# Kernel tuning notes

Hardware: AMD Instinct MI355X
Metric: run time of the kernel (lower is better)

## Reference

```python
import jax, jax.numpy as jnp
import numpy as np

# Single-device simulation of MoE down-proj GEMM + intra-node reduce-scatter.
# Leading axis R simulates the tensor-parallel ranks (K-shards); summing over R
# is the reduce part of the reduce-scatter.

def setup_inputs() -> dict:
    key = jax.random.key(0)
    k1, k2, k3, k4 = jax.random.split(key, 4)
    R, T, TOPK, Kp, E, H = 4, 2048, 2, 1024, 8, 4096
    intermediate_states = jax.random.normal(k1, (R, T * TOPK, Kp), dtype=jnp.float16)
    w = (jax.random.normal(k2, (R, E, Kp, H), dtype=jnp.float16) * jnp.float16(0.02))
    topk_ids = jax.random.randint(k3, (T, TOPK), 0, E, dtype=jnp.int32)
    tw = jax.random.uniform(k4, (T, TOPK), dtype=jnp.float32)
    topk_weight = tw / tw.sum(axis=-1, keepdims=True)
    return {"intermediate_states": intermediate_states, "w": w,
            "topk_ids": topk_ids, "topk_weight": topk_weight}


def reference(intermediate_states, w, topk_ids, topk_weight):
    # intermediate_states: [R, T*TOPK, Kp] fp16 (per-rank K-shard of expert act.)
    # w:                   [R, E, Kp, H]   fp16 (per-rank shard of down-proj)
    # topk_ids:            [T, TOPK] int32 expert assignment per token slot
    # topk_weight:         [T, TOPK] fp32  router weights
    R, MT, Kp = intermediate_states.shape
    E, H = w.shape[1], w.shape[3]
    T, TOPK = topk_ids.shape
    ids = topk_ids.reshape(-1)  # [MT]
    zero = jnp.zeros((), intermediate_states.dtype)
    acc = jnp.zeros((MT, H), dtype=jnp.float32)
    # Grouped GEMM expressed as dense masked GEMMs (E is small & fixed);
    # sum over r == reduce over tensor-parallel K-shards (reduce-scatter).
    for r in range(R):
        for e in range(E):
            xm = jnp.where((ids == e)[:, None], intermediate_states[r], zero)
            acc = acc + jnp.matmul(xm, w[r, e], preferred_element_type=jnp.float32)
    acc = acc * topk_weight.reshape(-1)[:, None]          # router weighting
    out = acc.reshape(T, TOPK, H).sum(axis=1)              # reduce topk per token
    return out.astype(intermediate_states.dtype)           # [T, H] fp16
```

## Files before the change

### kernel.cpp

```cpp
#include <hip/hip_runtime.h>
#include <stdint.h>

#define R_    4
#define T_    2048
#define TOPK_ 2
#define MT_   (T_ * TOPK_)
#define Kp_   1024
#define E_    8
#define H_    4096

#define BM 128
#define BN 128
#define BK 64
#define NKI 64
#define MAXT 40
#define NWG  (MAXT * (H_ / BN))

#define WS_TE    16
#define WS_TRS   80
#define WS_TNR   144
#define WS_RIDX  256
#define WS_X16_OFF   32768
#define WS_X16_BYTES ((size_t)R_ * MT_ * Kp_ * 2)
#define WS_NEEDED    (WS_X16_OFF + WS_X16_BYTES)

typedef _Float16 f16x8 __attribute__((ext_vector_type(8)));
typedef __fp16   h16x2 __attribute__((ext_vector_type(2)));
typedef float    f32x4 __attribute__((ext_vector_type(4)));
typedef float    f32x2 __attribute__((ext_vector_type(2)));

__device__ __forceinline__ void gload_lds16(const void* g, void* l) {
  __builtin_amdgcn_global_load_lds(
      (const __attribute__((address_space(1))) uint8_t*)g,
      (__attribute__((address_space(3))) uint8_t*)l, 16, 0, 0);
}

__global__ void moe_prep(const int* __restrict__ ids, int* __restrict__ ws) {
  __shared__ int cnt[E_], off[E_], cur[E_];
  const int tid = threadIdx.x;
  if (tid < E_) { cnt[tid] = 0; cur[tid] = 0; }
  __syncthreads();
  for (int m = tid; m < MT_; m += 256) atomicAdd(&cnt[ids[m]], 1);
  __syncthreads();
  if (tid == 0) {
    int o = 0, nt = 0;
    for (int e = 0; e < E_; ++e) {
      off[e] = o;
      int c = cnt[e];
      for (int t = 0; t < (c + 127) / 128; ++t) {
        ws[WS_TE + nt]  = e;
        ws[WS_TRS + nt] = o + t * 128;
        int rem = c - t * 128;
        ws[WS_TNR + nt] = rem < 128 ? rem : 128;
        ++nt;
      }
      o += c;
    }
    for (; nt < MAXT; ++nt) ws[WS_TNR + nt] = 0;
  }
  __syncthreads();
  for (int m = tid; m < MT_; m += 256) {
    int e = ids[m];
    int p = off[e] + atomicAdd(&cur[e], 1);
    ws[WS_RIDX + p] = m;
  }
}

__global__ void cvt_x(const float* __restrict__ x, _Float16* __restrict__ x16) {
  const size_t n = (size_t)R_ * MT_ * Kp_;
  size_t i = ((size_t)blockIdx.x * 256 + threadIdx.x) * 8;
  const size_t stride = (size_t)gridDim.x * 256 * 8;
  for (; i < n; i += stride) {
    f32x4 a = *(const f32x4*)(x + i);
    f32x4 b = *(const f32x4*)(x + i + 4);
    union { f16x8 v; h16x2 h[4]; } u;
    u.h[0] = __builtin_amdgcn_cvt_pkrtz(a[0], a[1]);
    u.h[1] = __builtin_amdgcn_cvt_pkrtz(a[2], a[3]);
    u.h[2] = __builtin_amdgcn_cvt_pkrtz(b[0], b[1]);
    u.h[3] = __builtin_amdgcn_cvt_pkrtz(b[2], b[3]);
    *(f16x8*)(x16 + i) = u.v;
  }
}

__global__ __launch_bounds__(512, 4) void moe_gemm_f(
    const _Float16* __restrict__ x16, const float* __restrict__ w,
    const float* __restrict__ tw, const int* __restrict__ ws,
    float* __restrict__ out)
{
  __shared__ __align__(16) char Alds[2][16384];
  __shared__ __align__(16) char Blds[2][16384];

  const int lid = blockIdx.x;
  const int swz = (lid & 7) * (NWG / 8) + (lid >> 3);
  const int bt  = swz % MAXT;
  const int h0  = (swz / MAXT) * BN;

  const int nr = ws[WS_TNR + bt];
  if (nr == 0) return;
  const int e  = ws[WS_TE + bt];
  const int rs = ws[WS_TRS + bt];
  const int* __restrict__ ridx = ws + WS_RIDX;

  const int tid = threadIdx.x;
  const int wv  = tid >> 6;
  const int ln  = tid & 63;
  const int g   = ln >> 4;
  const int c16 = ln & 15;
  const int wr = wv >> 2, wc = wv & 3;

  uint32_t asrc[2];
#pragma unroll
  for (int i = 0; i < 2; ++i) {
    int q   = tid * 16 + i * 8192;
    int row = q >> 7;
    int col = (q & 127) ^ (((q >> 7) & 7) << 4);
    int rcl = row < nr ? row : nr - 1;
    asrc[i] = (uint32_t)ridx[rs + rcl] * (Kp_ * 2) + col;
  }

  const int p  = tid & 63;
  const int kh = tid >> 6;
  const int hr0 = 2 * p, hr1 = 2 * p + 1;
  const uint32_t bw0 = hr0 * 128 + ((kh * 16) ^ ((hr0 & 7) << 4));
  const uint32_t bw1 = hr1 * 128 + ((kh * 16) ^ ((hr1 & 7) << 4));

  uint32_t aoff[4][2], boff[2][2];
#pragma unroll
  for (int mi = 0; mi < 4; ++mi) {
    int row = wr * 64 + mi * 16 + c16;
#pragma unroll
    for (int ks = 0; ks < 2; ++ks)
      aoff[mi][ks] = row * 128 + ((ks * 64 + g * 16) ^ ((row & 7) << 4));
  }
#pragma unroll
  for (int ni = 0; ni < 2; ++ni) {
    int row = wc * 32 + ni * 16 + c16;
#pragma unroll
    for (int ks = 0; ks < 2; ++ks)
      boff[ni][ks] = row * 128 + ((ks * 64 + g * 16) ^ ((row & 7) << 4));
  }

  f32x4 acc[4][2];
#pragma unroll
  for (int mi = 0; mi < 4; ++mi)
#pragma unroll
    for (int ni = 0; ni < 2; ++ni)
      acc[mi][ni] = f32x4{0.f, 0.f, 0.f, 0.f};

  const char* xb = (const char*)x16;
  f32x2 bvE[8], bvO[8];

#define AISSUE(BUF_, KK_) do {                                              \
    const int r_ = (KK_) >> 4, kb_ = ((KK_) & 15) << 7;                     \
    const char* xk_ = xb + (size_t)r_ * (MT_ * Kp_ * 2) + kb_;              \
    _Pragma("unroll")                                                       \
    for (int i_ = 0; i_ < 2; ++i_)                                          \
      gload_lds16(xk_ + asrc[i_], Alds[BUF_] + i_ * 8192 + wv * 1024);      \
  } while (0)

#define BISSUE(BV_, KK_) do {                                               \
    const int r_ = (KK_) >> 4, kp_ = ((KK_) & 15) << 6;                     \
    const float* wk_ = w + (((size_t)(r_ * E_ + e)) * Kp_ + kp_) * H_ + h0; \
    _Pragma("unroll")                                                       \
    for (int i_ = 0; i_ < 8; ++i_)                                          \
      BV_[i_] = *(const f32x2*)(wk_ + (size_t)(kh * 8 + i_) * H_ + 2 * p);  \
  } while (0)

#define BWRITE(BV_, BUF_) do {                                              \
    union { f16x8 v; h16x2 h[4]; } lo_, hi_;                                \
    _Pragma("unroll")                                                       \
    for (int j_ = 0; j_ < 4; ++j_) {                                        \
      lo_.h[j_] = __builtin_amdgcn_cvt_pkrtz(BV_[2*j_][0], BV_[2*j_+1][0]); \
      hi_.h[j_] = __builtin_amdgcn_cvt_pkrtz(BV_[2*j_][1], BV_[2*j_+1][1]); \
    }                                                                       \
    *(f16x8*)(Blds[BUF_] + bw0) = lo_.v;                                    \
    *(f16x8*)(Blds[BUF_] + bw1) = hi_.v;                                    \
  } while (0)

#define COMPUTE_KS(BUF_, KS_) do {                                          \
    f16x8 af[4], bf[2];                                                     \
    _Pragma("unroll")                                                       \
    for (int mi = 0; mi < 4; ++mi)                                          \
      af[mi] = *(const f16x8*)(Alds[BUF_] + aoff[mi][KS_]);                 \
    _Pragma("unroll")                                                       \
    for (int ni = 0; ni < 2; ++ni)                                          \
      bf[ni] = *(const f16x8*)(Blds[BUF_] + boff[ni][KS_]);                 \
    __builtin_amdgcn_s_setprio(1);                                          \
    _Pragma("unroll")                                                       \
    for (int mi = 0; mi < 4; ++mi)                                          \
      _Pragma("unroll")                                                     \
      for (int ni = 0; ni < 2; ++ni)                                        \
        acc[mi][ni] = __builtin_amdgcn_mfma_f32_16x16x32_f16(               \
            af[mi], bf[ni], acc[mi][ni], 0, 0, 0);                          \
    __builtin_amdgcn_s_setprio(0);                                          \
  } while (0)

  BISSUE(bvE, 0);
  AISSUE(0, 0);
  BWRITE(bvE, 0);
  BISSUE(bvO, 1);
  asm volatile("s_waitcnt vmcnt(8)" ::: "memory");
  asm volatile("s_waitcnt lgkmcnt(0)" ::: "memory");
  __builtin_amdgcn_s_barrier();

  for (int kk = 0; kk <= NKI - 4; kk += 2) {
    __builtin_amdgcn_sched_barrier(0);
    COMPUTE_KS(0, 0);
    AISSUE(1, kk + 1);
    BISSUE(bvE, kk + 2);
    __builtin_amdgcn_sched_barrier(0);
    BWRITE(bvO, 1);
    COMPUTE_KS(0, 1);
    asm volatile("s_waitcnt vmcnt(8)" ::: "memory");
    asm volatile("s_waitcnt lgkmcnt(0)" ::: "memory");
    __builtin_amdgcn_s_barrier();
    __builtin_amdgcn_sched_barrier(0);
    COMPUTE_KS(1, 0);
    AISSUE(0, kk + 2);
    BISSUE(bvO, kk + 3);
    __builtin_amdgcn_sched_barrier(0);
    BWRITE(bvE, 0);
    COMPUTE_KS(1, 1);
    asm volatile("s_waitcnt vmcnt(8)" ::: "memory");
    asm volatile("s_waitcnt lgkmcnt(0)" ::: "memory");
    __builtin_amdgcn_s_barrier();
  }
  __builtin_amdgcn_sched_barrier(0);
  COMPUTE_KS(0, 0);
  AISSUE(1, NKI - 1);
  __builtin_amdgcn_sched_barrier(0);
  BWRITE(bvO, 1);
  COMPUTE_KS(0, 1);
  asm volatile("s_waitcnt vmcnt(0)" ::: "memory");
  asm volatile("s_waitcnt lgkmcnt(0)" ::: "memory");
  __builtin_amdgcn_s_barrier();
  __builtin_amdgcn_sched_barrier(0);
  COMPUTE_KS(1, 0);
  COMPUTE_KS(1, 1);

#undef AISSUE
#undef BISSUE
#undef BWRITE
#undef COMPUTE_KS

#pragma unroll
  for (int mi = 0; mi < 4; ++mi) {
#pragma unroll
    for (int jj = 0; jj < 4; ++jj) {
      int row = wr * 64 + mi * 16 + g * 4 + jj;
      if (row < nr) {
        int m   = ridx[rs + row];
        float twv = tw[m];
        int t = m >> 1;
        float* op = out + (size_t)t * H_ + h0 + wc * 32 + c16;
#pragma unroll
        for (int ni = 0; ni < 2; ++ni)
          atomicAdd(op + ni * 16, acc[mi][ni][jj] * twv);
      }
    }
  }
}

__global__ __launch_bounds__(256) void moe_gemm_fb(
    const float* __restrict__ x, const float* __restrict__ w,
    const float* __restrict__ tw, const int* __restrict__ ws,
    float* __restrict__ out)
{
  __shared__ __align__(16) char Alds[16384];
  __shared__ __align__(16) char Blds[16384];

  const int bt = blockIdx.x;
  const int nr = ws[WS_TNR + bt];
  if (nr == 0) return;
  const int e  = ws[WS_TE + bt];
  const int rs = ws[WS_TRS + bt];
  const int r  = blockIdx.y;
  const int h0 = blockIdx.z * 128;
  const int* __restrict__ ridx = ws + WS_RIDX;

  const int tid = threadIdx.x;
  const int wv  = tid >> 6;
  const int ln  = tid & 63;
  const int g   = ln >> 4;
  const int c16 = ln & 15;
  const int wr = wv >> 1, wc = wv & 1;

  size_t   asrc[4];
  uint32_t awr[4];
#pragma unroll
  for (int i = 0; i < 4; ++i) {
    int q   = (tid + i * 256) * 16;
    int row = q >> 7;
    int el0 = (q & 127) >> 1;
    int rcl = row < nr ? row : nr - 1;
    int slot = ridx[rs + rcl];
    asrc[i] = (size_t)slot * Kp_ + el0;
    awr[i]  = row * 128 + ((q & 127) ^ ((row & 7) << 4));
  }
  const int p  = tid & 63;
  const int kh = tid >> 6;
  const int hr0 = 2 * p, hr1 = 2 * p + 1;
  uint32_t bw[4];
#pragma unroll
  for (int q = 0; q < 2; ++q) {
    bw[q]     = hr0 * 128 + ((kh * 32 + q * 16) ^ ((hr0 & 7) << 4));
    bw[2 + q] = hr1 * 128 + ((kh * 32 + q * 16) ^ ((hr1 & 7) << 4));
  }
  uint32_t aoff[4][2], boff[4][2];
#pragma unroll
  for (int mi = 0; mi < 4; ++mi) {
    int row = wr * 64 + mi * 16 + c16;
#pragma unroll
    for (int ks = 0; ks < 2; ++ks)
      aoff[mi][ks] = row * 128 + ((ks * 64 + g * 16) ^ ((row & 7) << 4));
  }
#pragma unroll
  for (int ni = 0; ni < 4; ++ni) {
    int row = wc * 64 + ni * 16 + c16;
#pragma unroll
    for (int ks = 0; ks < 2; ++ks)
      boff[ni][ks] = row * 128 + ((ks * 64 + g * 16) ^ ((row & 7) << 4));
  }

  f32x4 acc[4][4];
#pragma unroll
  for (int mi = 0; mi < 4; ++mi)
#pragma unroll
    for (int ni = 0; ni < 4; ++ni)
      acc[mi][ni] = f32x4{0.f, 0.f, 0.f, 0.f};

  const float* xbase = x + (size_t)r * MT_ * Kp_;
  const float* wbase = w + ((size_t)(r * E_ + e) * Kp_) * (size_t)H_ + h0;

  for (int kk = 0; kk < Kp_ / 64; ++kk) {
    const float* xk = xbase + (kk << 6);
    const float* wk = wbase + (size_t)(kk << 6) * H_;
    f32x4 av0[4], av1[4];
    f32x2 bv[16];
#pragma unroll
    for (int i = 0; i < 4; ++i) {
      av0[i] = *(const f32x4*)(xk + asrc[i]);
      av1[i] = *(const f32x4*)(xk + asrc[i] + 4);
    }
#pragma unroll
    for (int i = 0; i < 16; ++i)
      bv[i] = *(const f32x2*)(wk + (size_t)(kh * 16 + i) * H_ + 2 * p);
    __syncthreads();
#pragma unroll
    for (int i = 0; i < 4; ++i) {
      union { f16x8 v; h16x2 h[4]; } u;
      u.h[0] = __builtin_amdgcn_cvt_pkrtz(av0[i][0], av0[i][1]);
      u.h[1] = __builtin_amdgcn_cvt_pkrtz(av0[i][2], av0[i][3]);
      u.h[2] = __builtin_amdgcn_cvt_pkrtz(av1[i][0], av1[i][1]);
      u.h[3] = __builtin_amdgcn_cvt_pkrtz(av1[i][2], av1[i][3]);
      *(f16x8*)(Alds + awr[i]) = u.v;
    }
#pragma unroll
    for (int q = 0; q < 2; ++q) {
      union { f16x8 v; h16x2 h[4]; } lo, hi;
#pragma unroll
      for (int j = 0; j < 4; ++j) {
        lo.h[j] = __builtin_amdgcn_cvt_pkrtz(bv[q * 8 + 2 * j][0], bv[q * 8 + 2 * j + 1][0]);
        hi.h[j] = __builtin_amdgcn_cvt_pkrtz(bv[q * 8 + 2 * j][1], bv[q * 8 + 2 * j + 1][1]);
      }
      *(f16x8*)(Blds + bw[q])     = lo.v;
      *(f16x8*)(Blds + bw[2 + q]) = hi.v;
    }
    __syncthreads();
#pragma unroll
    for (int ks = 0; ks < 2; ++ks) {
      f16x8 af[4], bf[4];
#pragma unroll
      for (int mi = 0; mi < 4; ++mi)
        af[mi] = *(const f16x8*)(Alds + aoff[mi][ks]);
#pragma unroll
      for (int ni = 0; ni < 4; ++ni)
        bf[ni] = *(const f16x8*)(Blds + boff[ni][ks]);
#pragma unroll
      for (int mi = 0; mi < 4; ++mi)
#pragma unroll
        for (int ni = 0; ni < 4; ++ni)
          acc[mi][ni] = __builtin_amdgcn_mfma_f32_16x16x32_f16(
              af[mi], bf[ni], acc[mi][ni], 0, 0, 0);
    }
  }

#pragma unroll
  for (int mi = 0; mi < 4; ++mi) {
#pragma unroll
    for (int jj = 0; jj < 4; ++jj) {
      int row = wr * 64 + mi * 16 + g * 4 + jj;
      if (row < nr) {
        int m   = ridx[rs + row];
        float twv = tw[m];
        int t = m >> 1;
        float* op = out + (size_t)t * H_ + h0 + wc * 64 + c16;
#pragma unroll
        for (int ni = 0; ni < 4; ++ni)
          atomicAdd(op + ni * 16, acc[mi][ni][jj] * twv);
      }
    }
  }
}

extern "C" void kernel_launch(void* const* d_in, const int* in_sizes, int n_in,
                              void* d_out, int out_size, void* d_ws, size_t ws_size,
                              hipStream_t stream) {
  const float* x   = (const float*)d_in[0];
  const float* w   = (const float*)d_in[1];
  const int*   ids = (const int*)d_in[2];
  const float* tw  = (const float*)d_in[3];
  float* out = (float*)d_out;
  int* ws = (int*)d_ws;

  (void)hipMemsetAsync(d_out, 0, (size_t)T_ * H_ * 4, stream);
  hipLaunchKernelGGL(moe_prep, dim3(1), dim3(256), 0, stream, ids, ws);

  if (ws_size >= WS_NEEDED) {
    _Float16* x16 = (_Float16*)((char*)d_ws + WS_X16_OFF);
    hipLaunchKernelGGL(cvt_x, dim3(2048), dim3(256), 0, stream, x, x16);
    hipLaunchKernelGGL(moe_gemm_f, dim3(NWG), dim3(512), 0, stream,
                       x16, w, tw, ws, out);
  } else {
    hipLaunchKernelGGL(moe_gemm_fb, dim3(MAXT, R_, H_ / 128), dim3(256), 0,
                       stream, x, w, tw, ws, out);
  }
}
```

Measured before the change: 378.0 us.

## Triple-buffer A tiles in LDS to prefetch two stages ahead and reswizzle B

Grows the A shared-memory buffer from two to three stages so the async global-to-LDS loads for A are issued two K-steps ahead, and restructures the main loop into a six-step unrolled rotation with a single barrier per K-step. The B LDS XOR swizzle now keys on row pairs instead of single rows, which is meant to cut bank conflicts on the paired B writes. The extra 16KB of LDS per workgroup may reduce occupancy, and the waitcnt thresholds were retuned to match the deeper pipeline.

```diff
diff --git a/kernel.cpp b/kernel.cpp
--- a/kernel.cpp
+++ b/kernel.cpp
@@ -87,7 +87,7 @@
     const float* __restrict__ tw, const int* __restrict__ ws,
     float* __restrict__ out)
 {
-  __shared__ __align__(16) char Alds[2][16384];
+  __shared__ __align__(16) char Alds[3][16384];
   __shared__ __align__(16) char Blds[2][16384];
 
   const int lid = blockIdx.x;
@@ -121,8 +121,9 @@
   const int p  = tid & 63;
   const int kh = tid >> 6;
   const int hr0 = 2 * p, hr1 = 2 * p + 1;
-  const uint32_t bw0 = hr0 * 128 + ((kh * 16) ^ ((hr0 & 7) << 4));
-  const uint32_t bw1 = hr1 * 128 + ((kh * 16) ^ ((hr1 & 7) << 4));
+  const uint32_t bslot = (uint32_t)((p & 7) << 4);
+  const uint32_t bw0 = hr0 * 128 + ((kh * 16) ^ bslot);
+  const uint32_t bw1 = hr1 * 128 + ((kh * 16) ^ bslot);
 
   uint32_t aoff[4][2], boff[2][2];
 #pragma unroll
@@ -137,7 +138,7 @@
     int row = wc * 32 + ni * 16 + c16;
 #pragma unroll
     for (int ks = 0; ks < 2; ++ks)
-      boff[ni][ks] = row * 128 + ((ks * 64 + g * 16) ^ ((row & 7) << 4));
+      boff[ni][ks] = row * 128 + ((ks * 64 + g * 16) ^ (((row >> 1) & 7) << 4));
   }
 
   f32x4 acc[4][2];
@@ -166,25 +167,25 @@
       BV_[i_] = *(const f32x2*)(wk_ + (size_t)(kh * 8 + i_) * H_ + 2 * p);  \
   } while (0)
 
-#define BWRITE(BV_, BUF_) do {                                              \
+#define BWRITE(BV_, BBUF_) do {                                             \
     union { f16x8 v; h16x2 h[4]; } lo_, hi_;                                \
     _Pragma("unroll")                                                       \
     for (int j_ = 0; j_ < 4; ++j_) {                                        \
       lo_.h[j_] = __builtin_amdgcn_cvt_pkrtz(BV_[2*j_][0], BV_[2*j_+1][0]); \
       hi_.h[j_] = __builtin_amdgcn_cvt_pkrtz(BV_[2*j_][1], BV_[2*j_+1][1]); \
     }                                                                       \
-    *(f16x8*)(Blds[BUF_] + bw0) = lo_.v;                                    \
-    *(f16x8*)(Blds[BUF_] + bw1) = hi_.v;                                    \
+    *(f16x8*)(Blds[BBUF_] + bw0) = lo_.v;                                   \
+    *(f16x8*)(Blds[BBUF_] + bw1) = hi_.v;                                   \
   } while (0)
 
-#define COMPUTE_KS(BUF_, KS_) do {                                          \
+#define COMPUTE_KS(ABUF_, BBUF_, KS_) do {                                  \
     f16x8 af[4], bf[2];                                                     \
     _Pragma("unroll")                                                       \
     for (int mi = 0; mi < 4; ++mi)                                          \
-      af[mi] = *(const f16x8*)(Alds[BUF_] + aoff[mi][KS_]);                 \
+      af[mi] = *(const f16x8*)(Alds[ABUF_] + aoff[mi][KS_]);                \
     _Pragma("unroll")                                                       \
     for (int ni = 0; ni < 2; ++ni)                                          \
-      bf[ni] = *(const f16x8*)(Blds[BUF_] + boff[ni][KS_]);                 \
+      bf[ni] = *(const f16x8*)(Blds[BBUF_] + boff[ni][KS_]);                \
     __builtin_amdgcn_s_setprio(1);                                          \
     _Pragma("unroll")                                                       \
     for (int mi = 0; mi < 4; ++mi)                                          \
@@ -195,53 +196,55 @@
     __builtin_amdgcn_s_setprio(0);                                          \
   } while (0)
 
+#define ITER_FULL(K_, AB_, AB2_, BB_, BVW_, BVI_) do {                      \
+    __builtin_amdgcn_sched_barrier(0);                                      \
+    COMPUTE_KS(AB_, BB_, 0);                                                \
+    AISSUE(AB2_, (K_) + 2);                                                 \
+    BISSUE(BVI_, (K_) + 2);                                                 \
+    __builtin_amdgcn_sched_barrier(0);                                      \
+    BWRITE(BVW_, (BB_) ^ 1);                                                \
+    COMPUTE_KS(AB_, BB_, 1);                                                \
+    asm volatile("s_waitcnt vmcnt(10)" ::: "memory");                       \
+    asm volatile("s_waitcnt lgkmcnt(0)" ::: "memory");                      \
+    __builtin_amdgcn_s_barrier();                                           \
+  } while (0)
+
   BISSUE(bvE, 0);
   AISSUE(0, 0);
+  AISSUE(1, 1);
+  BISSUE(bvO, 1);
   BWRITE(bvE, 0);
-  BISSUE(bvO, 1);
-  asm volatile("s_waitcnt vmcnt(8)" ::: "memory");
+  asm volatile("s_waitcnt vmcnt(10)" ::: "memory");
   asm volatile("s_waitcnt lgkmcnt(0)" ::: "memory");
   __builtin_amdgcn_s_barrier();
 
-  for (int kk = 0; kk <= NKI - 4; kk += 2) {
-    __builtin_amdgcn_sched_barrier(0);
-    COMPUTE_KS(0, 0);
-    AISSUE(1, kk + 1);
-    BISSUE(bvE, kk + 2);
-    __builtin_amdgcn_sched_barrier(0);
-    BWRITE(bvO, 1);
-    COMPUTE_KS(0, 1);
-    asm volatile("s_waitcnt vmcnt(8)" ::: "memory");
-    asm volatile("s_waitcnt lgkmcnt(0)" ::: "memory");
-    __builtin_amdgcn_s_barrier();
-    __builtin_amdgcn_sched_barrier(0);
-    COMPUTE_KS(1, 0);
-    AISSUE(0, kk + 2);
-    BISSUE(bvO, kk + 3);
-    __builtin_amdgcn_sched_barrier(0);
-    BWRITE(bvE, 0);
-    COMPUTE_KS(1, 1);
-    asm volatile("s_waitcnt vmcnt(8)" ::: "memory");
-    asm volatile("s_waitcnt lgkmcnt(0)" ::: "memory");
-    __builtin_amdgcn_s_barrier();
-  }
+  for (int kk = 0; kk < 60; kk += 6) {
+    ITER_FULL(kk + 0, 0, 2, 0, bvO, bvE);
+    ITER_FULL(kk + 1, 1, 0, 1, bvE, bvO);
+    ITER_FULL(kk + 2, 2, 1, 0, bvO, bvE);
+    ITER_FULL(kk + 3, 0, 2, 1, bvE, bvO);
+    ITER_FULL(kk + 4, 1, 0, 0, bvO, bvE);
+    ITER_FULL(kk + 5, 2, 1, 1, bvE, bvO);
+  }
+  ITER_FULL(60, 0, 2, 0, bvO, bvE);
+  ITER_FULL(61, 1, 0, 1, bvE, bvO);
   __builtin_amdgcn_sched_barrier(0);
-  COMPUTE_KS(0, 0);
-  AISSUE(1, NKI - 1);
+  COMPUTE_KS(2, 0, 0);
   __builtin_amdgcn_sched_barrier(0);
   BWRITE(bvO, 1);
-  COMPUTE_KS(0, 1);
+  COMPUTE_KS(2, 0, 1);
   asm volatile("s_waitcnt vmcnt(0)" ::: "memory");
   asm volatile("s_waitcnt lgkmcnt(0)" ::: "memory");
   __builtin_amdgcn_s_barrier();
   __builtin_amdgcn_sched_barrier(0);
-  COMPUTE_KS(1, 0);
-  COMPUTE_KS(1, 1);
+  COMPUTE_KS(0, 1, 0);
+  COMPUTE_KS(0, 1, 1);
 
 #undef AISSUE
 #undef BISSUE
 #undef BWRITE
 #undef COMPUTE_KS
+#undef ITER_FULL
 
 #pragma unroll
   for (int mi = 0; mi < 4; ++mi) {
```

Result: slower. 412.9 us (+9.2%).
